# Kernel tuning notes

Measured on AMD Instinct MI355X. Metric: run time of the kernel, lower is better.

Reference implementation:

```python
import jax, jax.numpy as jnp
import numpy as np

E = 8        # num_experts
TOP_K = 2

def setup_inputs() -> dict:
    key = jax.random.key(0)
    ks = jax.random.split(key, 5)
    B, T, D, F = 8, 2048, 1024, 2048
    s = 1.0 / np.sqrt(D)
    return {
        "x": jax.random.normal(ks[0], (B, T, D), dtype=jnp.float32),
        "gate_w": jax.random.normal(ks[1], (E, D), dtype=jnp.float32) * s,
        "w1": jax.random.normal(ks[2], (E, F, D), dtype=jnp.float32) * s,
        "w2": jax.random.normal(ks[3], (E, D, F), dtype=jnp.float32) * (1.0 / np.sqrt(F)),
        "w3": jax.random.normal(ks[4], (E, F, D), dtype=jnp.float32) * s,
    }

def _moe_forward(x, gate_w, w1, w2, w3):
    B, T, D = x.shape
    xf = x.reshape(-1, D)                                  # [N, D]
    logits = xf @ gate_w.T                                 # [N, E]
    probs = jax.nn.softmax(logits, axis=-1)                # [N, E]
    topk_p, topk_i = jax.lax.top_k(probs, TOP_K)           # [N, K]
    topk_p = topk_p / jnp.sum(topk_p, axis=-1, keepdims=True)
    # dense combine weights: [N, E], nonzero only at top-k experts
    onehot = jax.nn.one_hot(topk_i, E, dtype=xf.dtype)     # [N, K, E]
    cw = jnp.einsum("nk,nke->ne", topk_p, onehot)          # [N, E]
    out = jnp.zeros_like(xf)
    for e in range(E):  # small fixed expert count
        h = jax.nn.silu(xf @ w1[e].T) * (xf @ w3[e].T)     # [N, F]
        out = out + cw[:, e:e + 1] * (h @ w2[e].T)         # [N, D]
    return out.reshape(B, T, D)

def reference(x, gate_w, w1, w2, w3):
    return _moe_forward(x, gate_w, w1, w2, w3)
```

## Files before the change

### kernel.cpp

```cpp
#include <hip/hip_runtime.h>
#include <stdint.h>


typedef _Float16 f16;
typedef f16  f16x8 __attribute__((ext_vector_type(8)));
typedef f16  f16x4 __attribute__((ext_vector_type(4)));
typedef float fx4  __attribute__((ext_vector_type(4)));

#define NEXP 8
#define CHUNK 1024
#define M_PART 0
#define M_OFF  256
#define M_BB   272
#define M_TE   528
#define M_TR   1040

__device__ __forceinline__ void gload_lds16(const f16* g, f16* l) {
  __builtin_amdgcn_global_load_lds(
      (const __attribute__((address_space(1))) void*)g,
      (__attribute__((address_space(3))) void*)l, 16, 0, 0);
}

__global__ __launch_bounds__(256) void cvt_w13_kernel(const float* __restrict__ w1,
                                                      const float* __restrict__ w3,
                                                      f16* __restrict__ w13,
                                                      int D, int F, int FS, int fbase) {
  long i = (long)blockIdx.x * 256 + threadIdx.x;
  long n4 = (long)NEXP * 2 * FS * (D / 4);
  if (i >= n4) return;
  int d4 = (int)(i % (D / 4));
  int rr = (int)((i / (D / 4)) % (2 * FS));
  int e  = (int)(i / ((long)(D / 4) * 2 * FS));
  const float* src = ((rr & 1) ? w3 : w1) + ((long)e * F + fbase + (rr >> 1)) * D + d4 * 4;
  float4 v = *(const float4*)src;
  f16x4 o = {(f16)v.x, (f16)v.y, (f16)v.z, (f16)v.w};
  *(f16x4*)(w13 + i * 4) = o;
}

__global__ __launch_bounds__(256) void cvt_w2_kernel(const float* __restrict__ w2,
                                                     f16* __restrict__ w2s,
                                                     int D, int F, int FS, int fbase) {
  long i = (long)blockIdx.x * 256 + threadIdx.x;
  long n4 = (long)NEXP * D * (FS / 4);
  if (i >= n4) return;
  int k4 = (int)(i % (FS / 4));
  int d  = (int)((i / (FS / 4)) % D);
  int e  = (int)(i / ((long)(FS / 4) * D));
  const float* src = w2 + ((long)e * D + d) * F + fbase + k4 * 4;
  float4 v = *(const float4*)src;
  f16x4 o = {(f16)v.x, (f16)v.y, (f16)v.z, (f16)v.w};
  *(f16x4*)(w2s + i * 4) = o;
}

__global__ __launch_bounds__(256) void gate_kernel(const float* __restrict__ x,
                                                   const float* __restrict__ gw,
                                                   f16* __restrict__ xb,
                                                   int* __restrict__ topk_id,
                                                   float* __restrict__ topk_w,
                                                   int D) {
  const int lane = threadIdx.x & 63;
  const int wave = threadIdx.x >> 6;
  const long tok = (long)blockIdx.x * 4 + wave;
  const float* xrow = x + tok * D;

  float part[NEXP];
#pragma unroll
  for (int e = 0; e < NEXP; ++e) part[e] = 0.f;

  for (int c = 0; c < D / 256; ++c) {
    int idx = (c * 64 + lane) * 4;
    float4 xv = *(const float4*)(xrow + idx);
    f16x4 o = {(f16)xv.x, (f16)xv.y, (f16)xv.z, (f16)xv.w};
    *(f16x4*)(xb + tok * D + idx) = o;
#pragma unroll
    for (int e = 0; e < NEXP; ++e) {
      float4 gv = *(const float4*)(gw + (long)e * D + idx);
      part[e] += xv.x * gv.x + xv.y * gv.y + xv.z * gv.z + xv.w * gv.w;
    }
  }
#pragma unroll
  for (int e = 0; e < NEXP; ++e)
    for (int off = 32; off; off >>= 1) part[e] += __shfl_xor(part[e], off);

  int i0 = 0; float m0 = part[0];
#pragma unroll
  for (int e = 1; e < NEXP; ++e) if (part[e] > m0) { m0 = part[e]; i0 = e; }
  int i1 = (i0 == 0) ? 1 : 0; float m1 = part[i1];
#pragma unroll
  for (int e = 0; e < NEXP; ++e)
    if (e != i0 && e != ((i0 == 0) ? 1 : 0) && part[e] > m1) { m1 = part[e]; i1 = e; }

  if (lane == 0) {
    float w0 = 1.f / (1.f + expf(m1 - m0));
    float w1 = 1.f / (1.f + expf(m0 - m1));
    topk_id[2 * tok] = i0; topk_id[2 * tok + 1] = i1;
    topk_w[2 * tok] = w0;  topk_w[2 * tok + 1] = w1;
  }
}

__global__ __launch_bounds__(256) void count_kernel(const int* __restrict__ topk_id,
                                                    int* __restrict__ meta, int n2) {
  __shared__ int h[NEXP];
  const int t = threadIdx.x;
  if (t < NEXP) h[t] = 0;
  __syncthreads();
  const int lo = blockIdx.x * CHUNK;
  const int hi = min(n2, lo + CHUNK);
  for (int i = lo + t; i < hi; i += 256) atomicAdd(&h[topk_id[i]], 1);
  __syncthreads();
  if (t < NEXP) meta[M_PART + blockIdx.x * NEXP + t] = h[t];
}

__global__ void setup_kernel(int* __restrict__ meta, int* __restrict__ routed_token,
                             float* __restrict__ routed_w, int MT, int CB) {
  __shared__ int s_off[NEXP], s_cnt[NEXP];
  const int t = threadIdx.x;
  if (t == 0) {
    int cnt[NEXP];
    for (int e = 0; e < NEXP; ++e) cnt[e] = 0;
    for (int b = 0; b < CB; ++b)
      for (int e = 0; e < NEXP; ++e) cnt[e] += meta[M_PART + b * NEXP + e];
    int off = 0, tt = 0;
    for (int e = 0; e < NEXP; ++e) {
      s_cnt[e] = cnt[e]; s_off[e] = off;
      meta[M_OFF + e] = off;
      int p = (cnt[e] + 127) & ~127;
      for (int i = 0; i < (p >> 7); ++i) {
        meta[M_TE + tt] = e; meta[M_TR + tt] = off + i * 128; ++tt;
      }
      off += p;
    }
    meta[M_OFF + NEXP] = off;
    for (; tt < MT; ++tt) meta[M_TE + tt] = -1;
    for (int e = 0; e < NEXP; ++e) {
      int run = meta[M_OFF + e];
      for (int b = 0; b < CB; ++b) {
        meta[M_BB + b * NEXP + e] = run;
        run += meta[M_PART + b * NEXP + e];
      }
    }
  }
  __syncthreads();
  for (int e = 0; e < NEXP; ++e) {
    int start = s_off[e] + s_cnt[e];
    int end = s_off[e] + ((s_cnt[e] + 127) & ~127);
    for (int i = start + t; i < end; i += blockDim.x) {
      routed_token[i] = 0;
      routed_w[i] = 0.f;
    }
  }
}

__global__ __launch_bounds__(256) void scatter_kernel(const int* __restrict__ topk_id,
                                                      const float* __restrict__ topk_w,
                                                      const int* __restrict__ meta,
                                                      int* __restrict__ routed_token,
                                                      float* __restrict__ routed_w,
                                                      int* __restrict__ slot_pos,
                                                      int n2) {
  __shared__ int cur[NEXP];
  const int t = threadIdx.x;
  if (t < NEXP) cur[t] = meta[M_BB + blockIdx.x * NEXP + t];
  __syncthreads();
  const int lo = blockIdx.x * CHUNK;
  const int hi = min(n2, lo + CHUNK);
  for (int i = lo + t; i < hi; i += 256) {
    int e = topk_id[i];
    int pos = atomicAdd(&cur[e], 1);
    routed_token[pos] = i >> 1;
    routed_w[pos] = topk_w[i];
    slot_pos[i] = pos;
  }
}

__global__ __launch_bounds__(256) void ffn1_kernel(const f16* __restrict__ xb,
                                                   const f16* __restrict__ w13,
                                                   const int* __restrict__ routed_token,
                                                   const float* __restrict__ routed_w,
                                                   const int* __restrict__ meta,
                                                   f16* __restrict__ hbuf,
                                                   int D, int FS) {
  const int e = meta[M_TE + blockIdx.y];
  if (e < 0) return;
  const int r0 = meta[M_TR + blockIdx.y];
  const int f0 = blockIdx.x * 64;

  __shared__ __align__(16) f16 smem[2 * 128 * 64];
  __shared__ float s_w[128];
  f16* sA = smem;
  f16* sB = smem + 128 * 64;

  const int t = threadIdx.x;
  const int lane = t & 63;
  const int wave = t >> 6;
  const int wm = (wave & 1) * 64;
  const int wn = (wave >> 1) * 64;

  if (t < 128) s_w[t] = routed_w[r0 + t];

  const int rb = t >> 3;
  const int sgg = (t & 7) ^ (rb & 7);
  const f16* aptr[4];
  const f16* bptr[4];
#pragma unroll
  for (int q = 0; q < 4; ++q) {
    int r = q * 32 + rb;
    int tok = routed_token[r0 + r];
    aptr[q] = xb + (long)tok * D + sgg * 8;
    bptr[q] = w13 + ((long)e * 2 * FS + 2 * f0 + r) * D + sgg * 8;
  }
  f16* ldsA[4]; f16* ldsB[4];
#pragma unroll
  for (int q = 0; q < 4; ++q) {
    int gbase = (q * 256 + (t & ~63)) * 8;
    ldsA[q] = sA + gbase;
    ldsB[q] = sB + gbase;
  }

  fx4 acc[4][4];
#pragma unroll
  for (int i = 0; i < 4; ++i)
#pragma unroll
    for (int j = 0; j < 4; ++j) acc[i][j] = (fx4){0.f, 0.f, 0.f, 0.f};

  for (int kc = 0; kc < D; kc += 64) {
#pragma unroll
    for (int q = 0; q < 4; ++q) {
      gload_lds16(aptr[q] + kc, ldsA[q]);
      gload_lds16(bptr[q] + kc, ldsB[q]);
    }
    __syncthreads();
#pragma unroll
    for (int ks = 0; ks < 2; ++ks) {
      f16x8 aF[4], bF[4];
      const int kg = ks * 4 + (lane >> 4);
#pragma unroll
      for (int mf = 0; mf < 4; ++mf) {
        int row = wm + mf * 16 + (lane & 15);
        aF[mf] = *(const f16x8*)(sA + row * 64 + (kg ^ (row & 7)) * 8);
      }
#pragma unroll
      for (int nf = 0; nf < 4; ++nf) {
        int row = wn + nf * 16 + (lane & 15);
        bF[nf] = *(const f16x8*)(sB + row * 64 + (kg ^ (row & 7)) * 8);
      }
#pragma unroll
      for (int mf = 0; mf < 4; ++mf)
#pragma unroll
        for (int nf = 0; nf < 4; ++nf)
          acc[mf][nf] = __builtin_amdgcn_mfma_f32_16x16x32_f16(aF[mf], bF[nf], acc[mf][nf], 0, 0, 0);
    }
    __syncthreads();
  }

  f16* sH = smem;
  const int odd = lane & 1;
  const int j = (lane & 15) >> 1;
#pragma unroll
  for (int mf = 0; mf < 4; ++mf)
#pragma unroll
    for (int nfp = 0; nfp < 4; nfp += 2)
#pragma unroll
      for (int rg = 0; rg < 4; ++rg) {
        float v0 = acc[mf][nfp][rg];
        float v1 = acc[mf][nfp + 1][rg];
        float t0 = __shfl_xor(v0, 1);
        float t1 = __shfl_xor(v1, 1);
        float c1 = odd ? t1 : v0;
        float c3 = odd ? v1 : t0;
        float ex = __expf(-c1);
        float hv = c1 * c3 * __builtin_amdgcn_rcpf(1.f + ex);
        int ml = wm + mf * 16 + (lane >> 4) * 4 + rg;
        int fl = (wn >> 1) + (nfp + odd) * 8 + j;
        sH[ml * 72 + fl] = (f16)(hv * s_w[ml]);
      }
  __syncthreads();
#pragma unroll
  for (int q = 0; q < 4; ++q) {
    int gi = q * 256 + t;
    int r = gi >> 3, gc = gi & 7;
    *(f16x8*)(hbuf + (long)(r0 + r) * FS + f0 + gc * 8) = *(const f16x8*)(sH + r * 72 + gc * 8);
  }
}

__global__ __launch_bounds__(256) void ffn2_kernel(const f16* __restrict__ hbuf,
                                                   const f16* __restrict__ w2s,
                                                   const int* __restrict__ routed_token,
                                                   const int* __restrict__ meta,
                                                   float* __restrict__ out,
                                                   f16* __restrict__ ybuf,
                                                   int D, int FS) {
  const int e = meta[M_TE + blockIdx.y];
  if (e < 0) return;
  const int r0 = meta[M_TR + blockIdx.y];
  const int d0 = blockIdx.x * 128;

  __shared__ __align__(16) f16 smem[128 * 136];
  __shared__ int s_tok[128];
  f16* sA = smem;
  f16* sB = smem + 128 * 64;

  const int t = threadIdx.x;
  const int lane = t & 63;
  const int wave = t >> 6;
  const int wm = (wave & 1) * 64;
  const int wn = (wave >> 1) * 64;

  if (!ybuf && t < 128) s_tok[t] = routed_token[r0 + t];

  const int rb = t >> 3;
  const int sgg = (t & 7) ^ (rb & 7);
  const f16* aptr[4];
  const f16* bptr[4];
#pragma unroll
  for (int q = 0; q < 4; ++q) {
    int r = q * 32 + rb;
    aptr[q] = hbuf + (long)(r0 + r) * FS + sgg * 8;
    bptr[q] = w2s + ((long)e * D + d0 + r) * FS + sgg * 8;
  }
  f16* ldsA[4]; f16* ldsB[4];
#pragma unroll
  for (int q = 0; q < 4; ++q) {
    int gbase = (q * 256 + (t & ~63)) * 8;
    ldsA[q] = sA + gbase;
    ldsB[q] = sB + gbase;
  }

  fx4 acc[4][4];
#pragma unroll
  for (int i = 0; i < 4; ++i)
#pragma unroll
    for (int j = 0; j < 4; ++j) acc[i][j] = (fx4){0.f, 0.f, 0.f, 0.f};

  for (int kc = 0; kc < FS; kc += 64) {
#pragma unroll
    for (int q = 0; q < 4; ++q) {
      gload_lds16(aptr[q] + kc, ldsA[q]);
      gload_lds16(bptr[q] + kc, ldsB[q]);
    }
    __syncthreads();
#pragma unroll
    for (int ks = 0; ks < 2; ++ks) {
      f16x8 aF[4], bF[4];
      const int kg = ks * 4 + (lane >> 4);
#pragma unroll
      for (int mf = 0; mf < 4; ++mf) {
        int row = wm + mf * 16 + (lane & 15);
        aF[mf] = *(const f16x8*)(sA + row * 64 + (kg ^ (row & 7)) * 8);
      }
#pragma unroll
      for (int nf = 0; nf < 4; ++nf) {
        int row = wn + nf * 16 + (lane & 15);
        bF[nf] = *(const f16x8*)(sB + row * 64 + (kg ^ (row & 7)) * 8);
      }
#pragma unroll
      for (int mf = 0; mf < 4; ++mf)
#pragma unroll
        for (int nf = 0; nf < 4; ++nf)
          acc[mf][nf] = __builtin_amdgcn_mfma_f32_16x16x32_f16(aF[mf], bF[nf], acc[mf][nf], 0, 0, 0);
    }
    __syncthreads();
  }

  if (ybuf) {
    f16* sH = smem;
#pragma unroll
    for (int mf = 0; mf < 4; ++mf)
#pragma unroll
      for (int nf = 0; nf < 4; ++nf)
#pragma unroll
        for (int rg = 0; rg < 4; ++rg) {
          int row = wm + mf * 16 + (lane >> 4) * 4 + rg;
          int col = wn + nf * 16 + (lane & 15);
          sH[row * 136 + col] = (f16)acc[mf][nf][rg];
        }
    __syncthreads();
#pragma unroll
    for (int q = 0; q < 8; ++q) {
      int gi = q * 256 + t;
      int r = gi >> 4, c = (gi & 15) * 8;
      *(f16x8*)(ybuf + (long)(r0 + r) * D + d0 + c) = *(const f16x8*)(sH + r * 136 + c);
    }
  } else {
#pragma unroll
    for (int mf = 0; mf < 4; ++mf) {
#pragma unroll
      for (int rg = 0; rg < 4; ++rg) {
        int row = wm + mf * 16 + (lane >> 4) * 4 + rg;
        long obase = (long)s_tok[row] * D + d0;
#pragma unroll
        for (int nf = 0; nf < 4; ++nf) {
          int nl = wn + nf * 16 + (lane & 15);
          atomicAdd(out + obase + nl, acc[mf][nf][rg]);
        }
      }
    }
  }
}

__global__ __launch_bounds__(256) void combine_kernel(const f16* __restrict__ y,
                                                      const int* __restrict__ slot_pos,
                                                      float* __restrict__ out, int D) {
  const long tok = blockIdx.x;
  const int g = threadIdx.x * 8;
  const int p0 = slot_pos[2 * tok];
  const int p1 = slot_pos[2 * tok + 1];
  f16x8 a = *(const f16x8*)(y + (long)p0 * D + g);
  f16x8 b = *(const f16x8*)(y + (long)p1 * D + g);
  float* op = out + tok * D + g;
  float4 o0 = {(float)a[0] + (float)b[0], (float)a[1] + (float)b[1],
               (float)a[2] + (float)b[2], (float)a[3] + (float)b[3]};
  float4 o1 = {(float)a[4] + (float)b[4], (float)a[5] + (float)b[5],
               (float)a[6] + (float)b[6], (float)a[7] + (float)b[7]};
  *(float4*)op = o0;
  *(float4*)(op + 4) = o1;
}

extern "C" void kernel_launch(void* const* d_in, const int* in_sizes, int n_in,
                              void* d_out, int out_size, void* d_ws, size_t ws_size,
                              hipStream_t stream) {
  const float* x  = (const float*)d_in[0];
  const float* gw = (const float*)d_in[1];
  const float* w1 = (const float*)d_in[2];
  const float* w2 = (const float*)d_in[3];
  const float* w3 = (const float*)d_in[4];
  float* out = (float*)d_out;

  const int E = NEXP;
  const int D = in_sizes[1] / E;
  const long N = (long)in_sizes[0] / D;
  const int F = (int)((long)in_sizes[2] / ((long)E * D));
  const int MT = (int)(2 * N / 128 + E);
  const long RMAX = (long)MT * 128;
  const long out_bytes = (long)out_size * 4;
  const int n2 = (int)(2 * N);
  const int CB = (n2 + CHUNK - 1) / CHUNK;

  char* base = (char*)d_ws;
  long off = 0;
  int*   meta         = (int*)(base + off); off += 8 * 1024;
  int*   topk_id      = (int*)(base + off); off += 2 * N * 4;
  float* topk_w       = (float*)(base + off); off += 2 * N * 4;
  int*   slot_pos     = (int*)(base + off); off += 2 * N * 4;
  int*   routed_token = (int*)(base + off); off += RMAX * 4;
  float* routed_w     = (float*)(base + off); off += RMAX * 4;
  off = (off + 255) & ~255L;
  const long small_end = off;

  const long w13_b = (long)E * 2 * F * D * 2;
  const long xb_b  = N * (long)D * 2;

  int S = 0; bool w13_in_dout = false; bool use_y = false;
  f16 *xb = nullptr, *w2s = nullptr, *hbuf = nullptr, *ybuf = nullptr, *w13 = nullptr;
  int FS = F;

  if (out_bytes >= w13_b) {
    const long w2s_b  = (long)E * D * F * 2;
    const long hbuf_b = RMAX * (long)F * 2;
    const long ybuf_b = RMAX * (long)D * 2;
    const long ovl_b  = (xb_b > ybuf_b) ? xb_b : ybuf_b;
    if (small_end + w2s_b + hbuf_b + ovl_b <= (long)ws_size) {
      S = 1; w13_in_dout = true; use_y = true;
      long o = small_end;
      w2s  = (f16*)(base + o); o += w2s_b;
      hbuf = (f16*)(base + o); o += hbuf_b;
      xb   = (f16*)(base + o);
      ybuf = xb;
      w13  = (f16*)d_out;
    } else if (small_end + xb_b + w2s_b + hbuf_b <= (long)ws_size) {
      S = 1; w13_in_dout = true;
      long o = small_end;
      xb   = (f16*)(base + o); o += xb_b;
      w2s  = (f16*)(base + o); o += w2s_b;
      hbuf = (f16*)(base + o);
      w13  = (f16*)d_out;
    }
  }
  if (!S) {
    const int cands[4] = {2, 4, 8, 16};
    for (int ci = 0; ci < 4 && !S; ++ci) {
      int s = cands[ci];
      if (F % (64 * s)) continue;
      long FSl = F / s;
      long w2s_b  = (long)E * D * FSl * 2;
      long hbuf_b = RMAX * FSl * 2;
      long w13s_b = (long)E * 2 * FSl * D * 2;
      if (small_end + xb_b + w2s_b + hbuf_b + w13s_b <= (long)ws_size) {
        S = s; FS = (int)FSl;
        long o = small_end;
        xb   = (f16*)(base + o); o += xb_b;
        w2s  = (f16*)(base + o); o += w2s_b;
        hbuf = (f16*)(base + o); o += hbuf_b;
        w13  = (f16*)(base + o);
      }
    }
  }
  if (!S) return;

  hipMemsetAsync(meta, 0, 8 * 1024, stream);
  gate_kernel<<<(int)(N / 4), 256, 0, stream>>>(x, gw, xb, topk_id, topk_w, D);
  count_kernel<<<CB, 256, 0, stream>>>(topk_id, meta, n2);
  setup_kernel<<<1, 256, 0, stream>>>(meta, routed_token, routed_w, MT, CB);
  scatter_kernel<<<CB, 256, 0, stream>>>(topk_id, topk_w, meta, routed_token, routed_w,
                                         slot_pos, n2);

  const long n13 = (long)E * 2 * FS * (D / 4);
  const long nw2 = (long)E * D * (FS / 4);
  const int b13 = (int)((n13 + 255) / 256);
  const int bw2 = (int)((nw2 + 255) / 256);

  if (w13_in_dout) {
    cvt_w13_kernel<<<b13, 256, 0, stream>>>(w1, w3, w13, D, F, FS, 0);
    cvt_w2_kernel<<<bw2, 256, 0, stream>>>(w2, w2s, D, F, FS, 0);
    dim3 g1(FS / 64, MT);
    ffn1_kernel<<<g1, 256, 0, stream>>>(xb, w13, routed_token, routed_w, meta, hbuf, D, FS);
    dim3 g2(D / 128, MT);
    if (use_y) {
      ffn2_kernel<<<g2, 256, 0, stream>>>(hbuf, w2s, routed_token, meta, out, ybuf, D, FS);
      combine_kernel<<<(int)N, D / 8, 0, stream>>>(ybuf, slot_pos, out, D);
    } else {
      hipMemsetAsync(out, 0, out_bytes, stream);
      ffn2_kernel<<<g2, 256, 0, stream>>>(hbuf, w2s, routed_token, meta, out, nullptr, D, FS);
    }
  } else {
    hipMemsetAsync(out, 0, out_bytes, stream);
    for (int s = 0; s < S; ++s) {
      int fbase = s * FS;
      cvt_w13_kernel<<<b13, 256, 0, stream>>>(w1, w3, w13, D, F, FS, fbase);
      cvt_w2_kernel<<<bw2, 256, 0, stream>>>(w2, w2s, D, F, FS, fbase);
      dim3 g1(FS / 64, MT);
      ffn1_kernel<<<g1, 256, 0, stream>>>(xb, w13, routed_token, routed_w, meta, hbuf, D, FS);
      dim3 g2(D / 128, MT);
      ffn2_kernel<<<g2, 256, 0, stream>>>(hbuf, w2s, routed_token, meta, out, nullptr, D, FS);
    }
  }
}
```

Before: 922.8 us.

## Rewrite ffn1 as 256x256-tile, 8-wave, double-buffered pipelined MFMA GEMM

Rebuilds the gate/up expert GEMM with 256-row by 128-f (256 interleaved w1/w3 rows) tiles across 512 threads. LDS is double-buffered and global-to-LDS loads for the next k-step are interleaved with MFMA quadrants, using s_setprio and explicit barriers. New 256-row tile metadata with row limits is added to setup, and the routed buffers get padding. The aim is higher data reuse per LDS load and overlap of memory with compute. The cost is more LDS (128KB+) and registers per block, and more imbalance on partial 128-row tiles.

```diff
diff --git a/kernel.cpp b/kernel.cpp
--- a/kernel.cpp
+++ b/kernel.cpp
@@ -14,6 +14,9 @@
 #define M_BB   272
 #define M_TE   528
 #define M_TR   1040
+#define M_TE2  1552
+#define M_TR2  1696
+#define M_RL2  1840
 
 __device__ __forceinline__ void gload_lds16(const f16* g, f16* l) {
   __builtin_amdgcn_global_load_lds(
@@ -112,15 +115,15 @@
 }
 
 __global__ void setup_kernel(int* __restrict__ meta, int* __restrict__ routed_token,
-                             float* __restrict__ routed_w, int MT, int CB) {
-  __shared__ int s_off[NEXP], s_cnt[NEXP];
+                             float* __restrict__ routed_w, int MT, int MT2, int CB) {
+  __shared__ int s_off[NEXP], s_cnt[NEXP], s_tot;
   const int t = threadIdx.x;
   if (t == 0) {
     int cnt[NEXP];
     for (int e = 0; e < NEXP; ++e) cnt[e] = 0;
     for (int b = 0; b < CB; ++b)
       for (int e = 0; e < NEXP; ++e) cnt[e] += meta[M_PART + b * NEXP + e];
-    int off = 0, tt = 0;
+    int off = 0, tt = 0, t2 = 0;
     for (int e = 0; e < NEXP; ++e) {
       s_cnt[e] = cnt[e]; s_off[e] = off;
       meta[M_OFF + e] = off;
@@ -128,10 +131,18 @@
       for (int i = 0; i < (p >> 7); ++i) {
         meta[M_TE + tt] = e; meta[M_TR + tt] = off + i * 128; ++tt;
       }
+      int full = p >> 8;
+      for (int i = 0; i < full; ++i) {
+        meta[M_TE2 + t2] = e; meta[M_TR2 + t2] = off + i * 256; meta[M_RL2 + t2] = 256; ++t2;
+      }
+      if (p & 255) {
+        meta[M_TE2 + t2] = e; meta[M_TR2 + t2] = off + full * 256; meta[M_RL2 + t2] = 128; ++t2;
+      }
       off += p;
     }
-    meta[M_OFF + NEXP] = off;
+    meta[M_OFF + NEXP] = off; s_tot = off;
     for (; tt < MT; ++tt) meta[M_TE + tt] = -1;
+    for (; t2 < MT2; ++t2) meta[M_TE2 + t2] = -1;
     for (int e = 0; e < NEXP; ++e) {
       int run = meta[M_OFF + e];
       for (int b = 0; b < CB; ++b) {
@@ -148,6 +159,9 @@
       routed_token[i] = 0;
       routed_w[i] = 0.f;
     }
+  }
+  for (int i = s_tot + t; i < s_tot + 256; i += blockDim.x) {
+    routed_token[i] = 0; routed_w[i] = 0.f;
   }
 }
 
@@ -173,91 +187,133 @@
   }
 }
 
-__global__ __launch_bounds__(256) void ffn1_kernel(const f16* __restrict__ xb,
-                                                   const f16* __restrict__ w13,
-                                                   const int* __restrict__ routed_token,
-                                                   const float* __restrict__ routed_w,
-                                                   const int* __restrict__ meta,
-                                                   f16* __restrict__ hbuf,
-                                                   int D, int FS) {
-  const int e = meta[M_TE + blockIdx.y];
+#define STAGE_A(kk, h) do { int cc = (kk) & 1;                                  \
+    f16* d_ = smem + cc * 16384 + ((h) * 1024 + (t & ~63)) * 8;                 \
+    gload_lds16(aSrc[h][0] + (long)(kk) * 64, d_);                              \
+    gload_lds16(aSrc[h][1] + (long)(kk) * 64, d_ + 4096); } while (0)
+#define STAGE_B(kk, h) do { int cc = (kk) & 1;                                  \
+    f16* d_ = smem + 32768 + cc * 16384 + ((h) * 1024 + (t & ~63)) * 8;         \
+    gload_lds16(bSrc[h][0] + (long)(kk) * 64, d_);                              \
+    gload_lds16(bSrc[h][1] + (long)(kk) * 64, d_ + 4096); } while (0)
+#define READ_A(MH) do {                                                         \
+    _Pragma("unroll")                                                           \
+    for (int mf = 0; mf < 4; ++mf) {                                            \
+      _Pragma("unroll")                                                         \
+      for (int ks = 0; ks < 2; ++ks) {                                          \
+        int row = wr * 128 + (MH) * 64 + mf * 16 + rA;                          \
+        int kg = ks * 4 + kgb;                                                  \
+        aF[mf][ks] = *(const f16x8*)(Ab + row * 64 + ((kg ^ (row & 7)) * 8));   \
+      } } } while (0)
+#define READ_B(NH) do {                                                         \
+    _Pragma("unroll")                                                           \
+    for (int nf = 0; nf < 2; ++nf) {                                            \
+      _Pragma("unroll")                                                         \
+      for (int ks = 0; ks < 2; ++ks) {                                          \
+        int row = wc * 64 + ((NH) * 2 + nf) * 16 + rA;                          \
+        int kg = ks * 4 + kgb;                                                  \
+        bF[(NH) * 2 + nf][ks] = *(const f16x8*)(Bb + row * 64 + ((kg ^ (row & 7)) * 8)); \
+      } } } while (0)
+#define MFMA_Q(MH, NH) do {                                                     \
+    _Pragma("unroll")                                                           \
+    for (int mf = 0; mf < 4; ++mf) {                                            \
+      _Pragma("unroll")                                                         \
+      for (int nf = 0; nf < 2; ++nf) {                                          \
+        _Pragma("unroll")                                                       \
+        for (int ks = 0; ks < 2; ++ks) {                                        \
+          acc[(MH) * 4 + mf][(NH) * 2 + nf] = __builtin_amdgcn_mfma_f32_16x16x32_f16( \
+              aF[mf][ks], bF[(NH) * 2 + nf][ks], acc[(MH) * 4 + mf][(NH) * 2 + nf], 0, 0, 0); \
+        } } } } while (0)
+#define PH_MID() do { __builtin_amdgcn_s_barrier();                             \
+    asm volatile("s_waitcnt lgkmcnt(0)" ::: "memory");                          \
+    __builtin_amdgcn_sched_barrier(0);                                          \
+    __builtin_amdgcn_s_setprio(1); } while (0)
+#define PH_END() do { __builtin_amdgcn_s_setprio(0);                            \
+    __builtin_amdgcn_s_barrier();                                               \
+    __builtin_amdgcn_sched_barrier(0); } while (0)
+
+__global__ __launch_bounds__(512, 2) void ffn1_kernel(const f16* __restrict__ xb,
+                                                      const f16* __restrict__ w13,
+                                                      const int* __restrict__ routed_token,
+                                                      const float* __restrict__ routed_w,
+                                                      const int* __restrict__ meta,
+                                                      f16* __restrict__ hbuf,
+                                                      int D, int FS) {
+  const int e = meta[M_TE2 + blockIdx.y];
   if (e < 0) return;
-  const int r0 = meta[M_TR + blockIdx.y];
-  const int f0 = blockIdx.x * 64;
-
-  __shared__ __align__(16) f16 smem[2 * 128 * 64];
-  __shared__ float s_w[128];
-  f16* sA = smem;
-  f16* sB = smem + 128 * 64;
+  const int r0   = meta[M_TR2 + blockIdx.y];
+  const int rlim = meta[M_RL2 + blockIdx.y];
+  const int f0 = blockIdx.x * 128;
+
+  __shared__ __align__(16) f16 smem[4 * 256 * 64];
+  __shared__ float s_w[256];
 
   const int t = threadIdx.x;
   const int lane = t & 63;
   const int wave = t >> 6;
-  const int wm = (wave & 1) * 64;
-  const int wn = (wave >> 1) * 64;
-
-  if (t < 128) s_w[t] = routed_w[r0 + t];
-
-  const int rb = t >> 3;
-  const int sgg = (t & 7) ^ (rb & 7);
-  const f16* aptr[4];
-  const f16* bptr[4];
-#pragma unroll
-  for (int q = 0; q < 4; ++q) {
-    int r = q * 32 + rb;
-    int tok = routed_token[r0 + r];
-    aptr[q] = xb + (long)tok * D + sgg * 8;
-    bptr[q] = w13 + ((long)e * 2 * FS + 2 * f0 + r) * D + sgg * 8;
-  }
-  f16* ldsA[4]; f16* ldsB[4];
-#pragma unroll
-  for (int q = 0; q < 4; ++q) {
-    int gbase = (q * 256 + (t & ~63)) * 8;
-    ldsA[q] = sA + gbase;
-    ldsB[q] = sB + gbase;
-  }
-
-  fx4 acc[4][4];
-#pragma unroll
-  for (int i = 0; i < 4; ++i)
+  const int wr = wave >> 2;
+  const int wc = wave & 3;
+  const int rA = lane & 15;
+  const int kgb = lane >> 4;
+
+  if (t < 256) s_w[t] = routed_w[r0 + t];
+
+  const f16* aSrc[2][2];
+  const f16* bSrc[2][2];
+#pragma unroll
+  for (int h = 0; h < 2; ++h)
+#pragma unroll
+    for (int q = 0; q < 2; ++q) {
+      int gi = q * 512 + t;
+      int r = h * 128 + (gi >> 3);
+      int sg = (gi & 7) ^ (r & 7);
+      int tok = routed_token[r0 + r];
+      aSrc[h][q] = xb + (long)tok * D + sg * 8;
+      bSrc[h][q] = w13 + ((long)e * 2 * FS + 2 * f0 + r) * D + sg * 8;
+    }
+
+  fx4 acc[8][4];
+#pragma unroll
+  for (int i = 0; i < 8; ++i)
 #pragma unroll
     for (int j = 0; j < 4; ++j) acc[i][j] = (fx4){0.f, 0.f, 0.f, 0.f};
 
-  for (int kc = 0; kc < D; kc += 64) {
-#pragma unroll
-    for (int q = 0; q < 4; ++q) {
-      gload_lds16(aptr[q] + kc, ldsA[q]);
-      gload_lds16(bptr[q] + kc, ldsB[q]);
-    }
-    __syncthreads();
-#pragma unroll
-    for (int ks = 0; ks < 2; ++ks) {
-      f16x8 aF[4], bF[4];
-      const int kg = ks * 4 + (lane >> 4);
-#pragma unroll
-      for (int mf = 0; mf < 4; ++mf) {
-        int row = wm + mf * 16 + (lane & 15);
-        aF[mf] = *(const f16x8*)(sA + row * 64 + (kg ^ (row & 7)) * 8);
-      }
-#pragma unroll
-      for (int nf = 0; nf < 4; ++nf) {
-        int row = wn + nf * 16 + (lane & 15);
-        bF[nf] = *(const f16x8*)(sB + row * 64 + (kg ^ (row & 7)) * 8);
-      }
-#pragma unroll
-      for (int mf = 0; mf < 4; ++mf)
-#pragma unroll
-        for (int nf = 0; nf < 4; ++nf)
-          acc[mf][nf] = __builtin_amdgcn_mfma_f32_16x16x32_f16(aF[mf], bF[nf], acc[mf][nf], 0, 0, 0);
-    }
-    __syncthreads();
+  const int NT = D >> 6;
+
+  STAGE_B(0, 0); STAGE_B(0, 1);
+  STAGE_A(0, 0); STAGE_A(0, 1);
+  STAGE_B(1, 0); STAGE_B(1, 1);
+  asm volatile("s_waitcnt vmcnt(4)" ::: "memory");
+  __builtin_amdgcn_s_barrier();
+  __builtin_amdgcn_sched_barrier(0);
+
+  for (int k = 0; k < NT; ++k) {
+    const int c = k & 1;
+    const f16* Ab = smem + c * 16384;
+    const f16* Bb = smem + 32768 + c * 16384;
+    f16x8 aF[4][2], bF[4][2];
+    READ_A(0); READ_B(0);
+    if (k + 1 < NT) STAGE_A(k + 1, 0);
+    PH_MID(); MFMA_Q(0, 0); PH_END();
+    READ_B(1);
+    if (k + 1 < NT) STAGE_A(k + 1, 1);
+    PH_MID(); MFMA_Q(0, 1); PH_END();
+    READ_A(1);
+    if (k + 2 < NT) STAGE_B(k + 2, 0);
+    PH_MID(); MFMA_Q(1, 1); PH_END();
+    if (k + 2 < NT) STAGE_B(k + 2, 1);
+    __builtin_amdgcn_s_setprio(1);
+    MFMA_Q(1, 0);
+    __builtin_amdgcn_s_setprio(0);
+    asm volatile("s_waitcnt vmcnt(4)" ::: "memory");
+    __builtin_amdgcn_s_barrier();
+    __builtin_amdgcn_sched_barrier(0);
   }
 
   f16* sH = smem;
   const int odd = lane & 1;
   const int j = (lane & 15) >> 1;
 #pragma unroll
-  for (int mf = 0; mf < 4; ++mf)
+  for (int mf = 0; mf < 8; ++mf)
 #pragma unroll
     for (int nfp = 0; nfp < 4; nfp += 2)
 #pragma unroll
@@ -270,16 +326,18 @@
         float c3 = odd ? v1 : t0;
         float ex = __expf(-c1);
         float hv = c1 * c3 * __builtin_amdgcn_rcpf(1.f + ex);
-        int ml = wm + mf * 16 + (lane >> 4) * 4 + rg;
-        int fl = (wn >> 1) + (nfp + odd) * 8 + j;
-        sH[ml * 72 + fl] = (f16)(hv * s_w[ml]);
+        int ml = wr * 128 + mf * 16 + (lane >> 4) * 4 + rg;
+        int fl = wc * 32 + (nfp + odd) * 8 + j;
+        sH[ml * 136 + fl] = (f16)(hv * s_w[ml]);
       }
   __syncthreads();
 #pragma unroll
-  for (int q = 0; q < 4; ++q) {
-    int gi = q * 256 + t;
-    int r = gi >> 3, gc = gi & 7;
-    *(f16x8*)(hbuf + (long)(r0 + r) * FS + f0 + gc * 8) = *(const f16x8*)(sH + r * 72 + gc * 8);
+  for (int qq = 0; qq < 8; ++qq) {
+    int gi = qq * 512 + t;
+    int r = gi >> 4, gc = gi & 15;
+    if (r < rlim)
+      *(f16x8*)(hbuf + (long)(r0 + r) * FS + f0 + gc * 8) =
+          *(const f16x8*)(sH + r * 136 + gc * 8);
   }
 }
 
@@ -431,6 +489,7 @@
   const long N = (long)in_sizes[0] / D;
   const int F = (int)((long)in_sizes[2] / ((long)E * D));
   const int MT = (int)(2 * N / 128 + E);
+  const int MT2 = (int)(2 * N / 256 + E);
   const long RMAX = (long)MT * 128;
   const long out_bytes = (long)out_size * 4;
   const int n2 = (int)(2 * N);
@@ -442,8 +501,8 @@
   int*   topk_id      = (int*)(base + off); off += 2 * N * 4;
   float* topk_w       = (float*)(base + off); off += 2 * N * 4;
   int*   slot_pos     = (int*)(base + off); off += 2 * N * 4;
-  int*   routed_token = (int*)(base + off); off += RMAX * 4;
-  float* routed_w     = (float*)(base + off); off += RMAX * 4;
+  int*   routed_token = (int*)(base + off); off += (RMAX + 256) * 4;
+  float* routed_w     = (float*)(base + off); off += (RMAX + 256) * 4;
   off = (off + 255) & ~255L;
   const long small_end = off;
 
@@ -480,7 +539,7 @@
     const int cands[4] = {2, 4, 8, 16};
     for (int ci = 0; ci < 4 && !S; ++ci) {
       int s = cands[ci];
-      if (F % (64 * s)) continue;
+      if (F % (128 * s)) continue;
       long FSl = F / s;
       long w2s_b  = (long)E * D * FSl * 2;
       long hbuf_b = RMAX * FSl * 2;
@@ -500,7 +559,7 @@
   hipMemsetAsync(meta, 0, 8 * 1024, stream);
   gate_kernel<<<(int)(N / 4), 256, 0, stream>>>(x, gw, xb, topk_id, topk_w, D);
   count_kernel<<<CB, 256, 0, stream>>>(topk_id, meta, n2);
-  setup_kernel<<<1, 256, 0, stream>>>(meta, routed_token, routed_w, MT, CB);
+  setup_kernel<<<1, 256, 0, stream>>>(meta, routed_token, routed_w, MT, MT2, CB);
   scatter_kernel<<<CB, 256, 0, stream>>>(topk_id, topk_w, meta, routed_token, routed_w,
                                          slot_pos, n2);
 
@@ -512,8 +571,8 @@
   if (w13_in_dout) {
     cvt_w13_kernel<<<b13, 256, 0, stream>>>(w1, w3, w13, D, F, FS, 0);
     cvt_w2_kernel<<<bw2, 256, 0, stream>>>(w2, w2s, D, F, FS, 0);
-    dim3 g1(FS / 64, MT);
-    ffn1_kernel<<<g1, 256, 0, stream>>>(xb, w13, routed_token, routed_w, meta, hbuf, D, FS);
+    dim3 g1(FS / 128, MT2);
+    ffn1_kernel<<<g1, 512, 0, stream>>>(xb, w13, routed_token, routed_w, meta, hbuf, D, FS);
     dim3 g2(D / 128, MT);
     if (use_y) {
       ffn2_kernel<<<g2, 256, 0, stream>>>(hbuf, w2s, routed_token, meta, out, ybuf, D, FS);
@@ -528,8 +587,8 @@
       int fbase = s * FS;
       cvt_w13_kernel<<<b13, 256, 0, stream>>>(w1, w3, w13, D, F, FS, fbase);
       cvt_w2_kernel<<<bw2, 256, 0, stream>>>(w2, w2s, D, F, FS, fbase);
-      dim3 g1(FS / 64, MT);
-      ffn1_kernel<<<g1, 256, 0, stream>>>(xb, w13, routed_token, routed_w, meta, hbuf, D, FS);
+      dim3 g1(FS / 128, MT2);
+      ffn1_kernel<<<g1, 512, 0, stream>>>(xb, w13, routed_token, routed_w, meta, hbuf, D, FS);
       dim3 g2(D / 128, MT);
       ffn2_kernel<<<g2, 256, 0, stream>>>(hbuf, w2s, routed_token, meta, out, nullptr, D, FS);
     }
```

New measurement: 946.5 us. 2.6% more time.

## Pipeline expert GEMMs with double-buffered LDS, larger tiles and XCD swizzle

Applied to the files above, without the earlier changes.

Rewrites both expert FFN GEMM kernels to use 512-thread workgroups with 128x256 tiles, a K=32 double-buffered LDS pipeline that overlaps global-to-LDS loads with MFMA work, and s_setprio around the MFMA blocks. Launches become 1D with an XCD-aware block remapping, so neighbouring tiles share L2 on the same chiplet. Routed buffers are padded by 256 entries so the larger tiles can read past the end safely. The cost is more LDS per block and more registers per thread, plus a stricter F divisibility requirement.

```diff
diff --git a/kernel.cpp b/kernel.cpp
--- a/kernel.cpp
+++ b/kernel.cpp
@@ -19,6 +19,17 @@
   __builtin_amdgcn_global_load_lds(
       (const __attribute__((address_space(1))) void*)g,
       (__attribute__((address_space(3))) void*)l, 16, 0, 0);
+}
+
+__device__ __forceinline__ int xcd_swizzle(int orig, int nwg) {
+  int q = nwg >> 3, r = nwg & 7;
+  int xcd = orig & 7, idx = orig >> 3;
+  int base = (xcd < r) ? xcd * (q + 1) : r * (q + 1) + (xcd - r) * q;
+  return base + idx;
+}
+
+__device__ __forceinline__ int swz4(int g, int r) {
+  return g ^ ((r ^ (r >> 2)) & 3);
 }
 
 __global__ __launch_bounds__(256) void cvt_w13_kernel(const float* __restrict__ w1,
@@ -113,7 +124,7 @@
 
 __global__ void setup_kernel(int* __restrict__ meta, int* __restrict__ routed_token,
                              float* __restrict__ routed_w, int MT, int CB) {
-  __shared__ int s_off[NEXP], s_cnt[NEXP];
+  __shared__ int s_off[NEXP], s_cnt[NEXP], s_tot;
   const int t = threadIdx.x;
   if (t == 0) {
     int cnt[NEXP];
@@ -130,7 +141,7 @@
       }
       off += p;
     }
-    meta[M_OFF + NEXP] = off;
+    meta[M_OFF + NEXP] = off; s_tot = off;
     for (; tt < MT; ++tt) meta[M_TE + tt] = -1;
     for (int e = 0; e < NEXP; ++e) {
       int run = meta[M_OFF + e];
@@ -148,6 +159,9 @@
       routed_token[i] = 0;
       routed_w[i] = 0.f;
     }
+  }
+  for (int i = s_tot + t; i < s_tot + 256; i += blockDim.x) {
+    routed_token[i] = 0; routed_w[i] = 0.f;
   }
 }
 
@@ -173,48 +187,100 @@
   }
 }
 
-__global__ __launch_bounds__(256) void ffn1_kernel(const f16* __restrict__ xb,
-                                                   const f16* __restrict__ w13,
-                                                   const int* __restrict__ routed_token,
-                                                   const float* __restrict__ routed_w,
-                                                   const int* __restrict__ meta,
-                                                   f16* __restrict__ hbuf,
-                                                   int D, int FS) {
-  const int e = meta[M_TE + blockIdx.y];
+
+#define PIPE_LOOP(AB_READS, MFMA1, MFMA2)                                      \
+  for (int k = 0; k < NT; ++k) {                                               \
+    const f16* Ab = smem + (k & 1) * 4096;                                     \
+    const f16* Bb = smem + 8192 + (k & 1) * 8192;                              \
+    f16x8 aF[4], bF[4];                                                        \
+    AB_READS;                                                                  \
+    if (k + 1 < NT) STAGE_A(k + 1);                                            \
+    __builtin_amdgcn_s_barrier();                                              \
+    __builtin_amdgcn_s_setprio(1);                                             \
+    MFMA1;                                                                     \
+    __builtin_amdgcn_s_setprio(0);                                             \
+    asm volatile("s_waitcnt lgkmcnt(0)" ::: "memory");                         \
+    __builtin_amdgcn_s_barrier();                                              \
+    if (k + 2 < NT) STAGE_B(k + 2);                                            \
+    __builtin_amdgcn_s_setprio(1);                                             \
+    MFMA2;                                                                     \
+    __builtin_amdgcn_s_setprio(0);                                             \
+    if (k >= NT - 2) asm volatile("s_waitcnt vmcnt(0)" ::: "memory");          \
+    else             asm volatile("s_waitcnt vmcnt(2)" ::: "memory");          \
+    __builtin_amdgcn_s_barrier();                                              \
+  }
+
+#define STAGE_A(kk) gload_lds16(aSrc + (long)(kk) * 32,                        \
+                                smem + ((kk) & 1) * 4096 + (t & ~63) * 8)
+#define STAGE_B(kk) do {                                                       \
+    f16* d_ = smem + 8192 + ((kk) & 1) * 8192 + (t & ~63) * 8;                 \
+    gload_lds16(bSrc0 + (long)(kk) * 32, d_);                                  \
+    gload_lds16(bSrc1 + (long)(kk) * 32, d_ + 4096); } while (0)
+
+#define READS_AB do {                                                          \
+    _Pragma("unroll")                                                          \
+    for (int nf = 0; nf < 4; ++nf) {                                           \
+      int row = wc * 64 + nf * 16 + rA;                                        \
+      bF[nf] = *(const f16x8*)(Bb + row * 32 + swz4(kgb, row) * 8);            \
+    }                                                                          \
+    _Pragma("unroll")                                                          \
+    for (int mf = 0; mf < 4; ++mf) {                                           \
+      int row = wr * 64 + mf * 16 + rA;                                        \
+      aF[mf] = *(const f16x8*)(Ab + row * 32 + swz4(kgb, row) * 8);            \
+    } } while (0)
+
+#define MFMA_H(NLO) do {                                                       \
+    _Pragma("unroll")                                                          \
+    for (int mf = 0; mf < 4; ++mf) {                                           \
+      _Pragma("unroll")                                                        \
+      for (int nf = (NLO); nf < (NLO) + 2; ++nf)                               \
+        acc[mf][nf] = __builtin_amdgcn_mfma_f32_16x16x32_f16(                  \
+            aF[mf], bF[nf], acc[mf][nf], 0, 0, 0);                             \
+    } } while (0)
+
+#define PIPE_PROLOGUE do {                                                     \
+    STAGE_B(0); STAGE_A(0); STAGE_B(1);                                        \
+    asm volatile("s_waitcnt vmcnt(2)" ::: "memory");                           \
+    __builtin_amdgcn_s_barrier(); } while (0)
+
+__global__ __launch_bounds__(512, 4) void ffn1_kernel(const f16* __restrict__ xb,
+                                                      const f16* __restrict__ w13,
+                                                      const int* __restrict__ routed_token,
+                                                      const float* __restrict__ routed_w,
+                                                      const int* __restrict__ meta,
+                                                      f16* __restrict__ hbuf,
+                                                      int D, int FS) {
+  const int NX = FS >> 7;
+  const int wg = xcd_swizzle(blockIdx.x, gridDim.x);
+  const int bx = wg % NX, by = wg / NX;
+  const int e = meta[M_TE + by];
   if (e < 0) return;
-  const int r0 = meta[M_TR + blockIdx.y];
-  const int f0 = blockIdx.x * 64;
-
-  __shared__ __align__(16) f16 smem[2 * 128 * 64];
+  const int r0 = meta[M_TR + by];
+  const int f0 = bx * 128;
+
+  __shared__ __align__(16) f16 smem[24576];
   __shared__ float s_w[128];
-  f16* sA = smem;
-  f16* sB = smem + 128 * 64;
 
   const int t = threadIdx.x;
   const int lane = t & 63;
   const int wave = t >> 6;
-  const int wm = (wave & 1) * 64;
-  const int wn = (wave >> 1) * 64;
+  const int wr = wave >> 2;
+  const int wc = wave & 3;
+  const int rA = lane & 15;
+  const int kgb = lane >> 4;
 
   if (t < 128) s_w[t] = routed_w[r0 + t];
 
-  const int rb = t >> 3;
-  const int sgg = (t & 7) ^ (rb & 7);
-  const f16* aptr[4];
-  const f16* bptr[4];
-#pragma unroll
-  for (int q = 0; q < 4; ++q) {
-    int r = q * 32 + rb;
-    int tok = routed_token[r0 + r];
-    aptr[q] = xb + (long)tok * D + sgg * 8;
-    bptr[q] = w13 + ((long)e * 2 * FS + 2 * f0 + r) * D + sgg * 8;
-  }
-  f16* ldsA[4]; f16* ldsB[4];
-#pragma unroll
-  for (int q = 0; q < 4; ++q) {
-    int gbase = (q * 256 + (t & ~63)) * 8;
-    ldsA[q] = sA + gbase;
-    ldsB[q] = sB + gbase;
+  const f16* aSrc;
+  const f16* bSrc0;
+  const f16* bSrc1;
+  {
+    int r = t >> 2, sg = swz4(t & 3, r);
+    aSrc = xb + (long)routed_token[r0 + r] * D + sg * 8;
+    bSrc0 = w13 + ((long)e * 2 * FS + 2 * f0 + r) * D + sg * 8;
+    int r1 = 128 + r;
+    int sg1 = swz4(t & 3, r1);
+    bSrc1 = w13 + ((long)e * 2 * FS + 2 * f0 + r1) * D + sg1 * 8;
   }
 
   fx4 acc[4][4];
@@ -223,37 +289,12 @@
 #pragma unroll
     for (int j = 0; j < 4; ++j) acc[i][j] = (fx4){0.f, 0.f, 0.f, 0.f};
 
-  for (int kc = 0; kc < D; kc += 64) {
-#pragma unroll
-    for (int q = 0; q < 4; ++q) {
-      gload_lds16(aptr[q] + kc, ldsA[q]);
-      gload_lds16(bptr[q] + kc, ldsB[q]);
-    }
-    __syncthreads();
-#pragma unroll
-    for (int ks = 0; ks < 2; ++ks) {
-      f16x8 aF[4], bF[4];
-      const int kg = ks * 4 + (lane >> 4);
-#pragma unroll
-      for (int mf = 0; mf < 4; ++mf) {
-        int row = wm + mf * 16 + (lane & 15);
-        aF[mf] = *(const f16x8*)(sA + row * 64 + (kg ^ (row & 7)) * 8);
-      }
-#pragma unroll
-      for (int nf = 0; nf < 4; ++nf) {
-        int row = wn + nf * 16 + (lane & 15);
-        bF[nf] = *(const f16x8*)(sB + row * 64 + (kg ^ (row & 7)) * 8);
-      }
-#pragma unroll
-      for (int mf = 0; mf < 4; ++mf)
-#pragma unroll
-        for (int nf = 0; nf < 4; ++nf)
-          acc[mf][nf] = __builtin_amdgcn_mfma_f32_16x16x32_f16(aF[mf], bF[nf], acc[mf][nf], 0, 0, 0);
-    }
-    __syncthreads();
-  }
+  const int NT = D >> 5;
+  PIPE_PROLOGUE;
+  PIPE_LOOP(READS_AB, MFMA_H(0), MFMA_H(2));
 
   f16* sH = smem;
+  const int wm = wr * 64, wn = wc * 64;
   const int odd = lane & 1;
   const int j = (lane & 15) >> 1;
 #pragma unroll
@@ -272,58 +313,56 @@
         float hv = c1 * c3 * __builtin_amdgcn_rcpf(1.f + ex);
         int ml = wm + mf * 16 + (lane >> 4) * 4 + rg;
         int fl = (wn >> 1) + (nfp + odd) * 8 + j;
-        sH[ml * 72 + fl] = (f16)(hv * s_w[ml]);
+        sH[ml * 136 + fl] = (f16)(hv * s_w[ml]);
       }
   __syncthreads();
 #pragma unroll
-  for (int q = 0; q < 4; ++q) {
-    int gi = q * 256 + t;
-    int r = gi >> 3, gc = gi & 7;
-    *(f16x8*)(hbuf + (long)(r0 + r) * FS + f0 + gc * 8) = *(const f16x8*)(sH + r * 72 + gc * 8);
-  }
-}
-
-__global__ __launch_bounds__(256) void ffn2_kernel(const f16* __restrict__ hbuf,
-                                                   const f16* __restrict__ w2s,
-                                                   const int* __restrict__ routed_token,
-                                                   const int* __restrict__ meta,
-                                                   float* __restrict__ out,
-                                                   f16* __restrict__ ybuf,
-                                                   int D, int FS) {
-  const int e = meta[M_TE + blockIdx.y];
+  for (int qq = 0; qq < 4; ++qq) {
+    int gi = qq * 512 + t;
+    int r = gi >> 4, gc = gi & 15;
+    *(f16x8*)(hbuf + (long)(r0 + r) * FS + f0 + gc * 8) =
+        *(const f16x8*)(sH + r * 136 + gc * 8);
+  }
+}
+
+__global__ __launch_bounds__(512, 4) void ffn2_kernel(const f16* __restrict__ hbuf,
+                                                      const f16* __restrict__ w2s,
+                                                      const int* __restrict__ routed_token,
+                                                      const int* __restrict__ meta,
+                                                      float* __restrict__ out,
+                                                      f16* __restrict__ ybuf,
+                                                      int D, int FS) {
+  const int NX = D >> 8;
+  const int wg = xcd_swizzle(blockIdx.x, gridDim.x);
+  const int bx = wg % NX, by = wg / NX;
+  const int e = meta[M_TE + by];
   if (e < 0) return;
-  const int r0 = meta[M_TR + blockIdx.y];
-  const int d0 = blockIdx.x * 128;
-
-  __shared__ __align__(16) f16 smem[128 * 136];
+  const int r0 = meta[M_TR + by];
+  const int d0 = bx * 256;
+
+  __shared__ __align__(16) f16 smem[33792];
   __shared__ int s_tok[128];
-  f16* sA = smem;
-  f16* sB = smem + 128 * 64;
 
   const int t = threadIdx.x;
   const int lane = t & 63;
   const int wave = t >> 6;
-  const int wm = (wave & 1) * 64;
-  const int wn = (wave >> 1) * 64;
+  const int wr = wave >> 2;
+  const int wc = wave & 3;
+  const int rA = lane & 15;
+  const int kgb = lane >> 4;
 
   if (!ybuf && t < 128) s_tok[t] = routed_token[r0 + t];
 
-  const int rb = t >> 3;
-  const int sgg = (t & 7) ^ (rb & 7);
-  const f16* aptr[4];
-  const f16* bptr[4];
-#pragma unroll
-  for (int q = 0; q < 4; ++q) {
-    int r = q * 32 + rb;
-    aptr[q] = hbuf + (long)(r0 + r) * FS + sgg * 8;
-    bptr[q] = w2s + ((long)e * D + d0 + r) * FS + sgg * 8;
-  }
-  f16* ldsA[4]; f16* ldsB[4];
-#pragma unroll
-  for (int q = 0; q < 4; ++q) {
-    int gbase = (q * 256 + (t & ~63)) * 8;
-    ldsA[q] = sA + gbase;
-    ldsB[q] = sB + gbase;
+  const f16* aSrc;
+  const f16* bSrc0;
+  const f16* bSrc1;
+  {
+    int r = t >> 2, sg = swz4(t & 3, r);
+    aSrc = hbuf + (long)(r0 + r) * FS + sg * 8;
+    bSrc0 = w2s + ((long)e * D + d0 + r) * FS + sg * 8;
+    int r1 = 128 + r;
+    int sg1 = swz4(t & 3, r1);
+    bSrc1 = w2s + ((long)e * D + d0 + r1) * FS + sg1 * 8;
   }
 
   fx4 acc[4][4];
@@ -332,35 +371,9 @@
 #pragma unroll
     for (int j = 0; j < 4; ++j) acc[i][j] = (fx4){0.f, 0.f, 0.f, 0.f};
 
-  for (int kc = 0; kc < FS; kc += 64) {
-#pragma unroll
-    for (int q = 0; q < 4; ++q) {
-      gload_lds16(aptr[q] + kc, ldsA[q]);
-      gload_lds16(bptr[q] + kc, ldsB[q]);
-    }
-    __syncthreads();
-#pragma unroll
-    for (int ks = 0; ks < 2; ++ks) {
-      f16x8 aF[4], bF[4];
-      const int kg = ks * 4 + (lane >> 4);
-#pragma unroll
-      for (int mf = 0; mf < 4; ++mf) {
-        int row = wm + mf * 16 + (lane & 15);
-        aF[mf] = *(const f16x8*)(sA + row * 64 + (kg ^ (row & 7)) * 8);
-      }
-#pragma unroll
-      for (int nf = 0; nf < 4; ++nf) {
-        int row = wn + nf * 16 + (lane & 15);
-        bF[nf] = *(const f16x8*)(sB + row * 64 + (kg ^ (row & 7)) * 8);
-      }
-#pragma unroll
-      for (int mf = 0; mf < 4; ++mf)
-#pragma unroll
-        for (int nf = 0; nf < 4; ++nf)
-          acc[mf][nf] = __builtin_amdgcn_mfma_f32_16x16x32_f16(aF[mf], bF[nf], acc[mf][nf], 0, 0, 0);
-    }
-    __syncthreads();
-  }
+  const int NT = FS >> 5;
+  PIPE_PROLOGUE;
+  PIPE_LOOP(READS_AB, MFMA_H(0), MFMA_H(2));
 
   if (ybuf) {
     f16* sH = smem;
@@ -370,27 +383,28 @@
       for (int nf = 0; nf < 4; ++nf)
 #pragma unroll
         for (int rg = 0; rg < 4; ++rg) {
-          int row = wm + mf * 16 + (lane >> 4) * 4 + rg;
-          int col = wn + nf * 16 + (lane & 15);
-          sH[row * 136 + col] = (f16)acc[mf][nf][rg];
+          int row = wr * 64 + mf * 16 + (lane >> 4) * 4 + rg;
+          int col = wc * 64 + nf * 16 + (lane & 15);
+          sH[row * 264 + col] = (f16)acc[mf][nf][rg];
         }
     __syncthreads();
 #pragma unroll
-    for (int q = 0; q < 8; ++q) {
-      int gi = q * 256 + t;
-      int r = gi >> 4, c = (gi & 15) * 8;
-      *(f16x8*)(ybuf + (long)(r0 + r) * D + d0 + c) = *(const f16x8*)(sH + r * 136 + c);
+    for (int qq = 0; qq < 8; ++qq) {
+      int gi = qq * 512 + t;
+      int r = gi >> 5, gc = gi & 31;
+      *(f16x8*)(ybuf + (long)(r0 + r) * D + d0 + gc * 8) =
+          *(const f16x8*)(sH + r * 264 + gc * 8);
     }
   } else {
 #pragma unroll
     for (int mf = 0; mf < 4; ++mf) {
 #pragma unroll
       for (int rg = 0; rg < 4; ++rg) {
-        int row = wm + mf * 16 + (lane >> 4) * 4 + rg;
+        int row = wr * 64 + mf * 16 + (lane >> 4) * 4 + rg;
         long obase = (long)s_tok[row] * D + d0;
 #pragma unroll
         for (int nf = 0; nf < 4; ++nf) {
-          int nl = wn + nf * 16 + (lane & 15);
+          int nl = wc * 64 + nf * 16 + (lane & 15);
           atomicAdd(out + obase + nl, acc[mf][nf][rg]);
         }
       }
@@ -442,8 +456,8 @@
   int*   topk_id      = (int*)(base + off); off += 2 * N * 4;
   float* topk_w       = (float*)(base + off); off += 2 * N * 4;
   int*   slot_pos     = (int*)(base + off); off += 2 * N * 4;
-  int*   routed_token = (int*)(base + off); off += RMAX * 4;
-  float* routed_w     = (float*)(base + off); off += RMAX * 4;
+  int*   routed_token = (int*)(base + off); off += (RMAX + 256) * 4;
+  float* routed_w     = (float*)(base + off); off += (RMAX + 256) * 4;
   off = (off + 255) & ~255L;
   const long small_end = off;
 
@@ -480,7 +494,7 @@
     const int cands[4] = {2, 4, 8, 16};
     for (int ci = 0; ci < 4 && !S; ++ci) {
       int s = cands[ci];
-      if (F % (64 * s)) continue;
+      if (F % (128 * s)) continue;
       long FSl = F / s;
       long w2s_b  = (long)E * D * FSl * 2;
       long hbuf_b = RMAX * FSl * 2;
@@ -509,18 +523,19 @@
   const int b13 = (int)((n13 + 255) / 256);
   const int bw2 = (int)((nw2 + 255) / 256);
 
+  const int nwg1 = (FS / 128) * MT;
+  const int nwg2 = (D / 256) * MT;
+
   if (w13_in_dout) {
     cvt_w13_kernel<<<b13, 256, 0, stream>>>(w1, w3, w13, D, F, FS, 0);
     cvt_w2_kernel<<<bw2, 256, 0, stream>>>(w2, w2s, D, F, FS, 0);
-    dim3 g1(FS / 64, MT);
-    ffn1_kernel<<<g1, 256, 0, stream>>>(xb, w13, routed_token, routed_w, meta, hbuf, D, FS);
-    dim3 g2(D / 128, MT);
+    ffn1_kernel<<<nwg1, 512, 0, stream>>>(xb, w13, routed_token, routed_w, meta, hbuf, D, FS);
     if (use_y) {
-      ffn2_kernel<<<g2, 256, 0, stream>>>(hbuf, w2s, routed_token, meta, out, ybuf, D, FS);
+      ffn2_kernel<<<nwg2, 512, 0, stream>>>(hbuf, w2s, routed_token, meta, out, ybuf, D, FS);
       combine_kernel<<<(int)N, D / 8, 0, stream>>>(ybuf, slot_pos, out, D);
     } else {
       hipMemsetAsync(out, 0, out_bytes, stream);
-      ffn2_kernel<<<g2, 256, 0, stream>>>(hbuf, w2s, routed_token, meta, out, nullptr, D, FS);
+      ffn2_kernel<<<nwg2, 512, 0, stream>>>(hbuf, w2s, routed_token, meta, out, nullptr, D, FS);
     }
   } else {
     hipMemsetAsync(out, 0, out_bytes, stream);
@@ -528,10 +543,8 @@
       int fbase = s * FS;
       cvt_w13_kernel<<<b13, 256, 0, stream>>>(w1, w3, w13, D, F, FS, fbase);
       cvt_w2_kernel<<<bw2, 256, 0, stream>>>(w2, w2s, D, F, FS, fbase);
-      dim3 g1(FS / 64, MT);
-      ffn1_kernel<<<g1, 256, 0, stream>>>(xb, w13, routed_token, routed_w, meta, hbuf, D, FS);
-      dim3 g2(D / 128, MT);
-      ffn2_kernel<<<g2, 256, 0, stream>>>(hbuf, w2s, routed_token, meta, out, nullptr, D, FS);
-    }
-  }
-}
+      ffn1_kernel<<<nwg1, 512, 0, stream>>>(xb, w13, routed_token, routed_w, meta, hbuf, D, FS);
+      ffn2_kernel<<<nwg2, 512, 0, stream>>>(hbuf, w2s, routed_token, meta, out, nullptr, D, FS);
+    }
+  }
+}
```

Measured after the change: 859.5 us. -6.9%, faster.
